# Kernel tuning notes

Hardware: AMD Instinct MI355X
Metric: run time of the kernel (lower is better)

The kernel has to match this reference:

```python
import math
import jax, jax.numpy as jnp
import numpy as np

N_WIRES = 8
DIM = 2 ** N_WIRES  # 256-dim state vector


def _rx(state, w, theta):
    """Apply RX(theta) = exp(-i*theta*X/2) on wire w.
    state: (N, 2,2,...,2) complex; theta: scalar or (N,)."""
    st = jnp.moveaxis(state, w + 1, 1)          # (N, 2, rest...)
    a0, a1 = st[:, 0], st[:, 1]                 # (N, 2^7...)
    th = jnp.asarray(theta)
    c = jnp.cos(th / 2).astype(jnp.complex64)
    s = jnp.sin(th / 2).astype(jnp.complex64)
    if th.ndim == 1:  # per-sample angle: broadcast over remaining 7 wire axes
        c = c.reshape((-1,) + (1,) * (N_WIRES - 1))
        s = s.reshape((-1,) + (1,) * (N_WIRES - 1))
    n0 = c * a0 - 1j * s * a1
    n1 = -1j * s * a0 + c * a1
    st = jnp.stack([n0, n1], axis=1)
    return jnp.moveaxis(st, 1, w + 1)


def _cnot(state, cw, tw):
    """CNOT with control wire cw, target wire tw."""
    st = jnp.moveaxis(state, (cw + 1, tw + 1), (1, 2))  # (N, 2, 2, rest...)
    st = jnp.stack([st[:, 0], st[:, 1, ::-1]], axis=1)  # flip target where control=1
    return jnp.moveaxis(st, (1, 2), (cw + 1, tw + 1))


def _qlayer(h, params):
    """Batched 8-wire circuit: RX-encode, trainable RX, CNOT ring, <Z_w>.
    h: (N, 8) angles; params: (8,) trainable RX angles -> (N, 8) expectations."""
    n = h.shape[0]
    state = jnp.zeros((n, DIM), jnp.complex64).at[:, 0].set(1.0)
    state = state.reshape((n,) + (2,) * N_WIRES)
    for w in range(N_WIRES):
        state = _rx(state, w, h[:, w])
    for w in range(N_WIRES):
        state = _rx(state, w, params[w])
    for w in range(N_WIRES - 1):
        state = _cnot(state, w, w + 1)
    state = _cnot(state, N_WIRES - 1, 0)
    probs = jnp.real(state * jnp.conj(state))           # (N, 2,...,2)
    z = jnp.array([1.0, -1.0], jnp.float32)
    outs = []
    for w in range(N_WIRES):
        zw = z.reshape((1,) + (1,) * w + (2,) + (1,) * (N_WIRES - 1 - w))
        outs.append(jnp.sum(probs * zw, axis=tuple(range(1, N_WIRES + 1))))
    return jnp.stack(outs, axis=1)


def setup_inputs() -> dict:
    key = jax.random.key(0)
    k1, k2, k3, k4 = jax.random.split(key, 4)
    b, s, e = 4, 256, 256
    return {
        "x": jax.random.normal(k1, (b, s, e), jnp.float32),
        "q_params": jax.random.normal(k2, (8,), jnp.float32),
        "w_comb": jax.random.normal(k3, (e, e), jnp.float32) * (1.0 / math.sqrt(e)),
        "b_comb": jax.random.normal(k4, (e,), jnp.float32) * 0.01,
    }


def reference(x, q_params, w_comb, b_comb):
    b, s, e = x.shape
    heads, hd = 32, N_WIRES
    # quantum projection; q/k/v are three identical deterministic applications
    h = x.reshape(b * s * heads, hd)
    qkv = _qlayer(h, q_params).reshape(b, s, heads, hd)
    qh = jnp.transpose(qkv, (0, 2, 1, 3))               # (b, heads, s, hd)
    scores = jnp.einsum('bhqd,bhkd->bhqk', qh, qh) / math.sqrt(hd)
    attn = jax.nn.softmax(scores, axis=-1)              # dropout = identity (eval)
    out = jnp.einsum('bhqk,bhkd->bhqd', attn, qh)
    out = jnp.transpose(out, (0, 2, 1, 3)).reshape(b, s, e)
    return out @ w_comb.T + b_comb
```

## Files before the change

### kernel.cpp

```cpp
#include <hip/hip_runtime.h>
#include <math.h>


#define BATCH 4
#define SEQ   256
#define EMB   256
#define HEADS 32
#define HD    8

__global__ __launch_bounds__(512) void qattn_kernel(
    const float* __restrict__ x,
    const float* __restrict__ qp,
    float* __restrict__ att)
{
    const int blk   = blockIdx.x;
    const int qhalf = blk & 1;
    const int bh    = blk >> 1;
    const int b     = bh >> 5;
    const int h     = bh & 31;
    const int t     = threadIdx.x;
    const int r     = t & 127;
    const int kq    = t >> 7;

    __shared__ float k_lds[SEQ][HD];
    __shared__ float p_lds[3][128][12];

    if (t < SEQ) {
        const float* xr = x + ((size_t)(b * SEQ + t) * EMB + h * HD);
        float g[HD];
#pragma unroll
        for (int j = 0; j < HD; ++j) g[j] = cosf(xr[j] + qp[j]);
        float kv[HD];
        float run = g[0];
#pragma unroll
        for (int j = 1; j < HD; ++j) { run *= g[j]; kv[j] = run; }
        float s0 = g[1];
#pragma unroll
        for (int j = 2; j < HD; ++j) s0 *= g[j];
        kv[0] = s0;
        *reinterpret_cast<float4*>(&k_lds[t][0]) = make_float4(kv[0], kv[1], kv[2], kv[3]);
        *reinterpret_cast<float4*>(&k_lds[t][4]) = make_float4(kv[4], kv[5], kv[6], kv[7]);
    }
    __syncthreads();

    const int qrow = qhalf * 128 + r;
    float qs[HD];
    {
        const float c = 0.35355339059327373f * 1.4426950408889634f;
#pragma unroll
        for (int j = 0; j < HD; ++j) qs[j] = k_lds[qrow][j] * c;
    }

    float l  = 0.f;
    float a0 = 0.f, a1 = 0.f, a2 = 0.f, a3 = 0.f,
          a4 = 0.f, a5 = 0.f, a6 = 0.f, a7 = 0.f;

    const float* kb = &k_lds[kq * 64][0];
#pragma unroll 4
    for (int kk = 0; kk < 64; ++kk) {
        float4 kv0 = *reinterpret_cast<const float4*>(kb + kk * 8);
        float4 kv1 = *reinterpret_cast<const float4*>(kb + kk * 8 + 4);
        float d01 = fmaf(qs[1], kv0.y, qs[0] * kv0.x);
        float d23 = fmaf(qs[3], kv0.w, qs[2] * kv0.z);
        float d45 = fmaf(qs[5], kv1.y, qs[4] * kv1.x);
        float d67 = fmaf(qs[7], kv1.w, qs[6] * kv1.z);
        float d   = (d01 + d23) + (d45 + d67);
        float p   = exp2f(d);
        l += p;
        a0 = fmaf(p, kv0.x, a0); a1 = fmaf(p, kv0.y, a1);
        a2 = fmaf(p, kv0.z, a2); a3 = fmaf(p, kv0.w, a3);
        a4 = fmaf(p, kv1.x, a4); a5 = fmaf(p, kv1.y, a5);
        a6 = fmaf(p, kv1.z, a6); a7 = fmaf(p, kv1.w, a7);
    }

    if (kq) {
        float* pr = &p_lds[kq - 1][r][0];
        *reinterpret_cast<float4*>(pr + 0) = make_float4(l,  a0, a1, a2);
        *reinterpret_cast<float4*>(pr + 4) = make_float4(a3, a4, a5, a6);
        pr[8] = a7;
    }
    __syncthreads();
    if (kq == 0) {
#pragma unroll
        for (int qtr = 0; qtr < 3; ++qtr) {
            const float* pr = &p_lds[qtr][r][0];
            float4 v0 = *reinterpret_cast<const float4*>(pr + 0);
            float4 v1 = *reinterpret_cast<const float4*>(pr + 4);
            l  += v0.x;
            a0 += v0.y; a1 += v0.z; a2 += v0.w;
            a3 += v1.x; a4 += v1.y; a5 += v1.z; a6 += v1.w;
            a7 += pr[8];
        }
        const float inv = 1.0f / l;
        float* yr = att + ((size_t)(b * SEQ + qrow) * EMB + h * HD);
        *reinterpret_cast<float4*>(&yr[0]) = make_float4(a0 * inv, a1 * inv, a2 * inv, a3 * inv);
        *reinterpret_cast<float4*>(&yr[4]) = make_float4(a4 * inv, a5 * inv, a6 * inv, a7 * inv);
    }
}

#define BM2 32
#define BN2 32
#define BK2 128

__global__ __launch_bounds__(256) void comb_kernel(
    const float* __restrict__ A,
    const float* __restrict__ W,
    const float* __restrict__ bias,
    float* __restrict__ Y)
{
    __shared__ float AsT[BK2][BM2 + 2];
    __shared__ float WsT[BK2][BN2 + 2];

    const int tid  = threadIdx.x;
    const int row0 = blockIdx.x * BM2;
    const int col0 = blockIdx.y * BN2;

    const int tx = tid & 15;
    const int ty = tid >> 4;

    float acc00 = 0.f, acc01 = 0.f, acc10 = 0.f, acc11 = 0.f;

    const int r     = tid >> 3;
    const int cbase = (tid & 7) * 4;

    for (int k0 = 0; k0 < EMB; k0 += BK2) {
        const float* ar = A + (size_t)(row0 + r) * EMB + k0;
        const float* wr = W + (size_t)(col0 + r) * EMB + k0;
#pragma unroll
        for (int i = 0; i < 4; ++i) {
            const int c = cbase + i * 32;
            float4 av = *reinterpret_cast<const float4*>(&ar[c]);
            AsT[c + 0][r] = av.x; AsT[c + 1][r] = av.y;
            AsT[c + 2][r] = av.z; AsT[c + 3][r] = av.w;
            float4 wv = *reinterpret_cast<const float4*>(&wr[c]);
            WsT[c + 0][r] = wv.x; WsT[c + 1][r] = wv.y;
            WsT[c + 2][r] = wv.z; WsT[c + 3][r] = wv.w;
        }
        __syncthreads();

#pragma unroll 8
        for (int k = 0; k < BK2; ++k) {
            float2 a = *reinterpret_cast<const float2*>(&AsT[k][ty * 2]);
            float2 w = *reinterpret_cast<const float2*>(&WsT[k][tx * 2]);
            acc00 = fmaf(a.x, w.x, acc00); acc01 = fmaf(a.x, w.y, acc01);
            acc10 = fmaf(a.y, w.x, acc10); acc11 = fmaf(a.y, w.y, acc11);
        }
        __syncthreads();
    }

    const int colb = col0 + tx * 2;
    float2 bv = *reinterpret_cast<const float2*>(&bias[colb]);
    {
        const int row = row0 + ty * 2;
        *reinterpret_cast<float2*>(&Y[(size_t)row * EMB + colb]) =
            make_float2(acc00 + bv.x, acc01 + bv.y);
        *reinterpret_cast<float2*>(&Y[(size_t)(row + 1) * EMB + colb]) =
            make_float2(acc10 + bv.x, acc11 + bv.y);
    }
}

extern "C" void kernel_launch(void* const* d_in, const int* in_sizes, int n_in,
                              void* d_out, int out_size, void* d_ws, size_t ws_size,
                              hipStream_t stream) {
    const float* x    = (const float*)d_in[0];
    const float* qp   = (const float*)d_in[1];
    const float* w    = (const float*)d_in[2];
    const float* bias = (const float*)d_in[3];
    float* out = (float*)d_out;
    float* att = (float*)d_ws;

    qattn_kernel<<<BATCH * HEADS * 2, 512, 0, stream>>>(x, qp, att);
    comb_kernel<<<dim3((BATCH * SEQ) / BM2, EMB / BN2), 256, 0, stream>>>(att, w, bias, out);
}
```

Baseline: 75.65 us.

## Use packed FP32 FMA in attention and projection kernels, restructure LDS layouts

Both kernels switch to inline-asm v_pk_mul_f32/v_pk_fma_f32 on float pairs, so the dot products and accumulations issue fewer VALU instructions. The attention kernel also pads the per-row key LDS stride from 8 to 12 floats and uses the raw hardware exp2 builtin. The projection kernel now loads the full K=256 extent into LDS in one pass, with k-pairs interleaved per row, removing the second load and sync stage. In exchange it needs 64KB of LDS per block, which may limit occupancy, and the final reduction sums the two lanes of each pair.

Result: faster. 73.39 us (-3.0%).

```diff
diff --git a/kernel.cpp b/kernel.cpp
--- a/kernel.cpp
+++ b/kernel.cpp
@@ -7,6 +7,26 @@
 #define EMB   256
 #define HEADS 32
 #define HD    8
+
+typedef float v2f __attribute__((ext_vector_type(2)));
+typedef float v4f __attribute__((ext_vector_type(4)));
+
+static __device__ __forceinline__ v2f pk_fma(v2f a, v2f b, v2f c) {
+    v2f d;
+    asm("v_pk_fma_f32 %0, %1, %2, %3" : "=v"(d) : "v"(a), "v"(b), "v"(c));
+    return d;
+}
+static __device__ __forceinline__ v2f pk_mul(v2f a, v2f b) {
+    v2f d;
+    asm("v_pk_mul_f32 %0, %1, %2" : "=v"(d) : "v"(a), "v"(b));
+    return d;
+}
+
+#if __has_builtin(__builtin_amdgcn_exp2f)
+#define EXP2(xx) __builtin_amdgcn_exp2f(xx)
+#else
+#define EXP2(xx) exp2f(xx)
+#endif
 
 __global__ __launch_bounds__(512) void qattn_kernel(
     const float* __restrict__ x,
@@ -22,7 +42,7 @@
     const int r     = t & 127;
     const int kq    = t >> 7;
 
-    __shared__ float k_lds[SEQ][HD];
+    __shared__ float k_lds[SEQ][12];
     __shared__ float p_lds[3][128][12];
 
     if (t < SEQ) {
@@ -44,43 +64,51 @@
     __syncthreads();
 
     const int qrow = qhalf * 128 + r;
-    float qs[HD];
+    v2f q01, q23, q45, q67;
     {
         const float c = 0.35355339059327373f * 1.4426950408889634f;
-#pragma unroll
-        for (int j = 0; j < HD; ++j) qs[j] = k_lds[qrow][j] * c;
-    }
-
-    float l  = 0.f;
-    float a0 = 0.f, a1 = 0.f, a2 = 0.f, a3 = 0.f,
-          a4 = 0.f, a5 = 0.f, a6 = 0.f, a7 = 0.f;
+        float4 qv0 = *reinterpret_cast<const float4*>(&k_lds[qrow][0]);
+        float4 qv1 = *reinterpret_cast<const float4*>(&k_lds[qrow][4]);
+        q01 = (v2f){qv0.x * c, qv0.y * c};
+        q23 = (v2f){qv0.z * c, qv0.w * c};
+        q45 = (v2f){qv1.x * c, qv1.y * c};
+        q67 = (v2f){qv1.z * c, qv1.w * c};
+    }
+
+    float l = 0.f;
+    v2f A01 = {0.f, 0.f}, A23 = {0.f, 0.f}, A45 = {0.f, 0.f}, A67 = {0.f, 0.f};
 
     const float* kb = &k_lds[kq * 64][0];
 #pragma unroll 4
     for (int kk = 0; kk < 64; ++kk) {
-        float4 kv0 = *reinterpret_cast<const float4*>(kb + kk * 8);
-        float4 kv1 = *reinterpret_cast<const float4*>(kb + kk * 8 + 4);
-        float d01 = fmaf(qs[1], kv0.y, qs[0] * kv0.x);
-        float d23 = fmaf(qs[3], kv0.w, qs[2] * kv0.z);
-        float d45 = fmaf(qs[5], kv1.y, qs[4] * kv1.x);
-        float d67 = fmaf(qs[7], kv1.w, qs[6] * kv1.z);
-        float d   = (d01 + d23) + (d45 + d67);
-        float p   = exp2f(d);
+        float4 kv0 = *reinterpret_cast<const float4*>(kb + kk * 12);
+        float4 kv1 = *reinterpret_cast<const float4*>(kb + kk * 12 + 4);
+        v2f k01 = (v2f){kv0.x, kv0.y}, k23 = (v2f){kv0.z, kv0.w};
+        v2f k45 = (v2f){kv1.x, kv1.y}, k67 = (v2f){kv1.z, kv1.w};
+        v2f tt = pk_mul(q01, k01);
+        tt = pk_fma(q23, k23, tt);
+        tt = pk_fma(q45, k45, tt);
+        tt = pk_fma(q67, k67, tt);
+        float d = tt.x + tt.y;
+        float p = EXP2(d);
         l += p;
-        a0 = fmaf(p, kv0.x, a0); a1 = fmaf(p, kv0.y, a1);
-        a2 = fmaf(p, kv0.z, a2); a3 = fmaf(p, kv0.w, a3);
-        a4 = fmaf(p, kv1.x, a4); a5 = fmaf(p, kv1.y, a5);
-        a6 = fmaf(p, kv1.z, a6); a7 = fmaf(p, kv1.w, a7);
+        v2f pp = {p, p};
+        A01 = pk_fma(pp, k01, A01);
+        A23 = pk_fma(pp, k23, A23);
+        A45 = pk_fma(pp, k45, A45);
+        A67 = pk_fma(pp, k67, A67);
     }
 
     if (kq) {
         float* pr = &p_lds[kq - 1][r][0];
-        *reinterpret_cast<float4*>(pr + 0) = make_float4(l,  a0, a1, a2);
-        *reinterpret_cast<float4*>(pr + 4) = make_float4(a3, a4, a5, a6);
-        pr[8] = a7;
+        *reinterpret_cast<float4*>(pr + 0) = make_float4(l,     A01.x, A01.y, A23.x);
+        *reinterpret_cast<float4*>(pr + 4) = make_float4(A23.y, A45.x, A45.y, A67.x);
+        pr[8] = A67.y;
     }
     __syncthreads();
     if (kq == 0) {
+        float a0 = A01.x, a1 = A01.y, a2 = A23.x, a3 = A23.y;
+        float a4 = A45.x, a5 = A45.y, a6 = A67.x, a7 = A67.y;
 #pragma unroll
         for (int qtr = 0; qtr < 3; ++qtr) {
             const float* pr = &p_lds[qtr][r][0];
@@ -98,64 +126,65 @@
     }
 }
 
-#define BM2 32
-#define BN2 32
-#define BK2 128
-
 __global__ __launch_bounds__(256) void comb_kernel(
     const float* __restrict__ A,
     const float* __restrict__ W,
     const float* __restrict__ bias,
     float* __restrict__ Y)
 {
-    __shared__ float AsT[BK2][BM2 + 2];
-    __shared__ float WsT[BK2][BN2 + 2];
+    __shared__ float As2[128 * 64];
+    __shared__ float Ws2[128 * 64];
 
     const int tid  = threadIdx.x;
-    const int row0 = blockIdx.x * BM2;
-    const int col0 = blockIdx.y * BN2;
+    const int row0 = blockIdx.x * BATCH * HD;
+    const int col0 = blockIdx.y * 32;
+
+    {
+        const int r  = tid >> 3;
+        const int cb = (tid & 7) * 4;
+        const float* ar = A + (size_t)(row0 + r) * EMB;
+        const float* wr = W + (size_t)(col0 + r) * EMB;
+        const int mbase = (r >> 1) * 4 + (r & 1) * 2;
+#pragma unroll
+        for (int i = 0; i < 8; ++i) {
+            const int c  = cb + i * 32;
+            const int k2 = c >> 1;
+            float4 av = *reinterpret_cast<const float4*>(&ar[c]);
+            *reinterpret_cast<float2*>(&As2[k2 * 64 + mbase])       = make_float2(av.x, av.y);
+            *reinterpret_cast<float2*>(&As2[(k2 + 1) * 64 + mbase]) = make_float2(av.z, av.w);
+            float4 wv = *reinterpret_cast<const float4*>(&wr[c]);
+            *reinterpret_cast<float2*>(&Ws2[k2 * 64 + mbase])       = make_float2(wv.x, wv.y);
+            *reinterpret_cast<float2*>(&Ws2[(k2 + 1) * 64 + mbase]) = make_float2(wv.z, wv.w);
+        }
+    }
+    __syncthreads();
 
     const int tx = tid & 15;
     const int ty = tid >> 4;
 
-    float acc00 = 0.f, acc01 = 0.f, acc10 = 0.f, acc11 = 0.f;
-
-    const int r     = tid >> 3;
-    const int cbase = (tid & 7) * 4;
-
-    for (int k0 = 0; k0 < EMB; k0 += BK2) {
-        const float* ar = A + (size_t)(row0 + r) * EMB + k0;
-        const float* wr = W + (size_t)(col0 + r) * EMB + k0;
-#pragma unroll
-        for (int i = 0; i < 4; ++i) {
-            const int c = cbase + i * 32;
-            float4 av = *reinterpret_cast<const float4*>(&ar[c]);
-            AsT[c + 0][r] = av.x; AsT[c + 1][r] = av.y;
-            AsT[c + 2][r] = av.z; AsT[c + 3][r] = av.w;
-            float4 wv = *reinterpret_cast<const float4*>(&wr[c]);
-            WsT[c + 0][r] = wv.x; WsT[c + 1][r] = wv.y;
-            WsT[c + 2][r] = wv.z; WsT[c + 3][r] = wv.w;
-        }
-        __syncthreads();
-
+    v2f c00 = {0.f, 0.f}, c01 = {0.f, 0.f}, c10 = {0.f, 0.f}, c11 = {0.f, 0.f};
+
+    const float* ab = &As2[ty * 4];
+    const float* wb = &Ws2[tx * 4];
 #pragma unroll 8
-        for (int k = 0; k < BK2; ++k) {
-            float2 a = *reinterpret_cast<const float2*>(&AsT[k][ty * 2]);
-            float2 w = *reinterpret_cast<const float2*>(&WsT[k][tx * 2]);
-            acc00 = fmaf(a.x, w.x, acc00); acc01 = fmaf(a.x, w.y, acc01);
-            acc10 = fmaf(a.y, w.x, acc10); acc11 = fmaf(a.y, w.y, acc11);
-        }
-        __syncthreads();
-    }
+    for (int k2 = 0; k2 < 128; ++k2) {
+        v4f a4 = *reinterpret_cast<const v4f*>(ab + k2 * 64);
+        v4f w4 = *reinterpret_cast<const v4f*>(wb + k2 * 64);
+        c00 = pk_fma(a4.xy, w4.xy, c00);
+        c01 = pk_fma(a4.xy, w4.zw, c01);
+        c10 = pk_fma(a4.zw, w4.xy, c10);
+        c11 = pk_fma(a4.zw, w4.zw, c11);
+    }
+    __syncthreads();
 
     const int colb = col0 + tx * 2;
     float2 bv = *reinterpret_cast<const float2*>(&bias[colb]);
     {
         const int row = row0 + ty * 2;
         *reinterpret_cast<float2*>(&Y[(size_t)row * EMB + colb]) =
-            make_float2(acc00 + bv.x, acc01 + bv.y);
+            make_float2(c00.x + c00.y + bv.x, c01.x + c01.y + bv.y);
         *reinterpret_cast<float2*>(&Y[(size_t)(row + 1) * EMB + colb]) =
-            make_float2(acc10 + bv.x, acc11 + bv.y);
+            make_float2(c10.x + c10.y + bv.x, c11.x + c11.y + bv.y);
     }
 }
 
@@ -170,5 +199,5 @@
     float* att = (float*)d_ws;
 
     qattn_kernel<<<BATCH * HEADS * 2, 512, 0, stream>>>(x, qp, att);
-    comb_kernel<<<dim3((BATCH * SEQ) / BM2, EMB / BN2), 256, 0, stream>>>(att, w, bias, out);
-}
+    comb_kernel<<<dim3((BATCH * SEQ) / 32, EMB / 32), 256, 0, stream>>>(att, w, bias, out);
+}
```
